# Performance work log

Measured on AMD Instinct MI355X. Metric: run time of the kernel, lower is better.

Reference implementation:

```python
import jax, jax.numpy as jnp
import numpy as np

GROUPS = 32
HEADS = 8
EPS = 1e-5


def setup_inputs() -> dict:
    key = jax.random.key(0)
    ks = jax.random.split(key, 3)
    b, c, h, w = 8, 512, 32, 32
    x = jax.random.normal(ks[0], (b, c, h, w), dtype=jnp.float32)
    gn_w = jnp.ones((c,), jnp.float32)
    gn_b = jnp.zeros((c,), jnp.float32)
    qkv_w = jax.random.normal(ks[1], (3 * c, c), dtype=jnp.float32) * (1.0 / np.sqrt(c))
    qkv_b = jnp.zeros((3 * c,), jnp.float32)
    proj_w = jax.random.normal(ks[2], (c, c), dtype=jnp.float32) * (1.0 / np.sqrt(c))
    proj_b = jnp.zeros((c,), jnp.float32)
    return {"x": x, "gn_w": gn_w, "gn_b": gn_b, "qkv_w": qkv_w,
            "qkv_b": qkv_b, "proj_w": proj_w, "proj_b": proj_b}


def group_norm(x, weight, bias):
    b, c, h, w = x.shape
    xg = x.reshape(b, GROUPS, c // GROUPS, h, w)
    mean = xg.mean(axis=(2, 3, 4), keepdims=True)
    var = xg.var(axis=(2, 3, 4), keepdims=True)
    xn = ((xg - mean) * jax.lax.rsqrt(var + EPS)).reshape(b, c, h, w)
    return xn * weight[None, :, None, None] + bias[None, :, None, None]


def reference(x, gn_w, gn_b, qkv_w, qkv_b, proj_w, proj_b):
    b, c, h, w = x.shape
    dh = c // HEADS
    xn = group_norm(x, gn_w, gn_b)
    # 1x1 conv == per-pixel linear: (b,c,h,w) x (3c,c) -> (b,3c,h,w)
    qkv = jnp.einsum('bchw,oc->bohw', xn, qkv_w) + qkv_b[None, :, None, None]
    qkv = qkv.reshape(b, 3, HEADS, dh, h * w)  # 'three' outermost, then heads, head_dim
    q, k, v = qkv[:, 0], qkv[:, 1], qkv[:, 2]  # (b, heads, dh, hw)
    scale = dh ** (-0.5)
    attn = jax.nn.softmax(jnp.einsum('bhci,bhcj->bhij', q, k) * scale, axis=-1)
    out = jnp.einsum('bhij,bhcj->bhci', attn, v)  # (b, heads, dh, hw)
    out = out.reshape(b, c, h, w)
    out = jnp.einsum('bchw,oc->bohw', out, proj_w) + proj_b[None, :, None, None]
    return x + out
```

## Files before the change

### kernel.cpp

```cpp
#include <hip/hip_runtime.h>
#include <cstdint>
#include <cstddef>

#define BATCH 8
#define CCH   512
#define SSP   1024
#define NH    8
#define DH    64
#define O3    1536

typedef __bf16 bf16x8 __attribute__((ext_vector_type(8)));
typedef float  f32x4  __attribute__((ext_vector_type(4)));

__device__ __forceinline__ unsigned short f2bf(float f) {
    unsigned u = __builtin_bit_cast(unsigned, f);
    unsigned r = u + 0x7fffu + ((u >> 16) & 1u);
    return (unsigned short)(r >> 16);
}

__device__ __forceinline__ unsigned pk2bf(float lo, float hi) {
    unsigned ul = __builtin_bit_cast(unsigned, lo) + 0x8000u;
    unsigned uh = __builtin_bit_cast(unsigned, hi) + 0x8000u;
    return __builtin_amdgcn_perm(uh, ul, 0x07060302u);
}

__device__ __forceinline__ bf16x8 ld8(const unsigned short* p) {
    uint4 u = *(const uint4*)p;
    return __builtin_bit_cast(bf16x8, u);
}

__device__ __forceinline__ void glls16(const void* g, void* l) {
    __builtin_amdgcn_global_load_lds(
        (const __attribute__((address_space(1))) unsigned*)g,
        (__attribute__((address_space(3))) unsigned*)l, 16, 0, 0);
}

__global__ __launch_bounds__(256) void gn_wconv(const float* __restrict__ x,
                                                const float* __restrict__ gw,
                                                const float* __restrict__ gb,
                                                unsigned short* __restrict__ xnt,
                                                const float* __restrict__ s1,
                                                unsigned short* __restrict__ d1, int n1,
                                                const float* __restrict__ s2,
                                                unsigned short* __restrict__ d2) {
    int t = threadIdx.x;
    if (blockIdx.x >= 256) {
        int i = (blockIdx.x - 256) * 256 + t;
        const float4* sp;
        ushort4* dp;
        if (i < n1) { sp = (const float4*)s1 + i; dp = (ushort4*)d1 + i; }
        else        { sp = (const float4*)s2 + (i - n1); dp = (ushort4*)d2 + (i - n1); }
        float4 v = *sp;
        ushort4 o;
        o.x = f2bf(v.x); o.y = f2bf(v.y); o.z = f2bf(v.z); o.w = f2bf(v.w);
        *dp = o;
        return;
    }

    int blk = blockIdx.x;
    int b = blk >> 5, g = blk & 31;
    const float4* xp = (const float4*)(x + (size_t)(b * CCH + g * 16) * SSP);

    float4 vals[16];
    float sum = 0.f, ss = 0.f;
#pragma unroll
    for (int i = 0; i < 16; i++) {
        float4 v = xp[i * 256 + t];
        vals[i] = v;
        sum += (v.x + v.y) + (v.z + v.w);
        ss  += (v.x * v.x + v.y * v.y) + (v.z * v.z + v.w * v.w);
    }
#pragma unroll
    for (int o = 32; o; o >>= 1) {
        sum += __shfl_xor(sum, o, 64);
        ss  += __shfl_xor(ss,  o, 64);
    }
    __shared__ float red[8];
    if ((t & 63) == 0) { red[(t >> 6) * 2] = sum; red[(t >> 6) * 2 + 1] = ss; }
    __syncthreads();
    sum = red[0] + red[2] + red[4] + red[6];
    ss  = red[1] + red[3] + red[5] + red[7];

    float mean = sum * (1.f / 16384.f);
    float var  = ss * (1.f / 16384.f) - mean * mean;
    float rstd = rsqrtf(var + 1e-5f);

    __shared__ unsigned short tile[16][1032];
#pragma unroll
    for (int i = 0; i < 16; i++) {
        int f4 = i * 256 + t;
        int c = f4 >> 8;
        int s = (f4 & 255) * 4;
        float wsc = gw[g * 16 + c] * rstd;
        float bia = gb[g * 16 + c] - mean * wsc;
        float4 v = vals[i];
        tile[c][s + 0] = f2bf(v.x * wsc + bia);
        tile[c][s + 1] = f2bf(v.y * wsc + bia);
        tile[c][s + 2] = f2bf(v.z * wsc + bia);
        tile[c][s + 3] = f2bf(v.w * wsc + bia);
    }
    __syncthreads();

    int c2 = (t & 7) * 2, sr = t >> 3;
    unsigned short* outbase = xnt + (size_t)b * SSP * CCH + g * 16 + c2;
#pragma unroll
    for (int i = 0; i < 32; i++) {
        int s = i * 32 + sr;
        unsigned v = (unsigned)tile[c2][s] | ((unsigned)tile[c2 + 1][s] << 16);
        *(unsigned*)(outbase + (size_t)s * CCH) = v;
    }
}

__global__ __launch_bounds__(256) void gemm_qkv(const unsigned short* __restrict__ Aall,
                                                const unsigned short* __restrict__ Bw,
                                                const float* __restrict__ bias,
                                                unsigned short* __restrict__ Call,
                                                unsigned short* __restrict__ vtout) {
    const int K = 512;
    int bz = blockIdx.z;
    const unsigned short* A = Aall + (size_t)bz * SSP * CCH;
    int m0 = blockIdx.x * 128, n0 = blockIdx.y * 128;

    __shared__ unsigned short As[128 * 64], Bs[128 * 64];
    int t = threadIdx.x, wave = t >> 6, lane = t & 63;
    int quad = lane >> 4, l16 = lane & 15;
    int wm = (wave & 1) * 64, wn = (wave >> 1) * 64;

    int lrow = lane >> 3;
    int lc   = ((lane & 7) - lrow) & 7;
    const unsigned short* Ag = A  + (size_t)(m0 + wave * 32 + lrow) * K + lc * 8;
    const unsigned short* Bg = Bw + (size_t)(n0 + wave * 32 + lrow) * K + lc * 8;
    unsigned short* Asw = As + wave * 2048;
    unsigned short* Bsw = Bs + wave * 2048;

    f32x4 acc[4][4];
#pragma unroll
    for (int i = 0; i < 4; i++)
#pragma unroll
        for (int j = 0; j < 4; j++) acc[i][j] = f32x4{0.f, 0.f, 0.f, 0.f};

    int rowA = (wm + l16) * 64, rowB = (wn + l16) * 64;
    int cph[2];
#pragma unroll
    for (int kc = 0; kc < 2; kc++) cph[kc] = ((quad + 4 * kc + l16) & 7) * 8;

    for (int k0 = 0; k0 < K; k0 += 64) {
        __syncthreads();
#pragma unroll
        for (int i = 0; i < 4; i++) {
            glls16(Ag + (size_t)i * 8 * K + k0, Asw + i * 512);
            glls16(Bg + (size_t)i * 8 * K + k0, Bsw + i * 512);
        }
        __syncthreads();
#pragma unroll
        for (int kc = 0; kc < 2; kc++) {
            bf16x8 af[4], bfr[4];
#pragma unroll
            for (int i = 0; i < 4; i++) {
                af[i]  = ld8(As + rowA + i * 1024 + cph[kc]);
                bfr[i] = ld8(Bs + rowB + i * 1024 + cph[kc]);
            }
#pragma unroll
            for (int i = 0; i < 4; i++)
#pragma unroll
                for (int j = 0; j < 4; j++)
                    acc[i][j] = __builtin_amdgcn_mfma_f32_16x16x32_bf16(af[i], bfr[j], acc[i][j], 0, 0, 0);
        }
    }

    if (n0 < 1024) {
        float scl = (n0 < 512) ? 0.18033688011f : 1.0f;
        unsigned short* Cp = Call + (size_t)bz * SSP * O3;
#pragma unroll
        for (int i = 0; i < 4; i++)
#pragma unroll
            for (int j = 0; j < 4; j++) {
                int col = n0 + wn + j * 16 + l16;
                float bv = bias[col];
#pragma unroll
                for (int r = 0; r < 4; r++) {
                    int row = m0 + wm + i * 16 + quad * 4 + r;
                    Cp[(size_t)row * O3 + col] = f2bf((acc[i][j][r] + bv) * scl);
                }
            }
    } else {
#pragma unroll
        for (int j = 0; j < 4; j++) {
            int col = n0 + wn + j * 16 + l16;
            float bv = bias[col];
            unsigned short* vp = vtout + ((size_t)bz * 512 + (col - 1024)) * SSP;
#pragma unroll
            for (int i = 0; i < 4; i++) {
                int s = m0 + wm + i * 16 + quad * 4;
                uint2 d;
                d.x = pk2bf(acc[i][j][0] + bv, acc[i][j][1] + bv);
                d.y = pk2bf(acc[i][j][2] + bv, acc[i][j][3] + bv);
                *(uint2*)(vp + s) = d;
            }
        }
    }
}

__global__ __launch_bounds__(256) void gemm_proj(const unsigned short* __restrict__ Pw,
                                                 const unsigned short* __restrict__ Oall,
                                                 const float* __restrict__ bias,
                                                 const float* __restrict__ xres,
                                                 float* __restrict__ Out) {
    const int K = 512;
    int bz = blockIdx.z;
    const unsigned short* Bv = Oall + (size_t)bz * SSP * CCH;
    int m0 = blockIdx.x * 64, n0 = blockIdx.y * 128;

    __shared__ unsigned short As[64 * 64], Bs[128 * 64];
    int t = threadIdx.x, wave = t >> 6, lane = t & 63;
    int quad = lane >> 4, l16 = lane & 15;
    int wr = (wave & 1) * 32, wc = (wave >> 1) * 64;

    int lrow = lane >> 3;
    int lc   = ((lane & 7) - lrow) & 7;
    const unsigned short* Ag = Pw + (size_t)(m0 + wave * 16 + lrow) * K + lc * 8;
    const unsigned short* Bg = Bv + (size_t)(n0 + wave * 32 + lrow) * K + lc * 8;
    unsigned short* Asw = As + wave * 1024;
    unsigned short* Bsw = Bs + wave * 2048;

    f32x4 acc[2][4];
#pragma unroll
    for (int i = 0; i < 2; i++)
#pragma unroll
        for (int j = 0; j < 4; j++) acc[i][j] = f32x4{0.f, 0.f, 0.f, 0.f};

    int rowA = (wr + l16) * 64, rowB = (wc + l16) * 64;
    int cph[2];
#pragma unroll
    for (int kc = 0; kc < 2; kc++) cph[kc] = ((quad + 4 * kc + l16) & 7) * 8;

    for (int k0 = 0; k0 < K; k0 += 64) {
        __syncthreads();
#pragma unroll
        for (int i = 0; i < 2; i++)
            glls16(Ag + (size_t)i * 8 * K + k0, Asw + i * 512);
#pragma unroll
        for (int i = 0; i < 4; i++)
            glls16(Bg + (size_t)i * 8 * K + k0, Bsw + i * 512);
        __syncthreads();
#pragma unroll
        for (int kc = 0; kc < 2; kc++) {
            bf16x8 af[2], bfr[4];
#pragma unroll
            for (int i = 0; i < 2; i++) af[i]  = ld8(As + rowA + i * 1024 + cph[kc]);
#pragma unroll
            for (int j = 0; j < 4; j++) bfr[j] = ld8(Bs + rowB + j * 1024 + cph[kc]);
#pragma unroll
            for (int i = 0; i < 2; i++)
#pragma unroll
                for (int j = 0; j < 4; j++)
                    acc[i][j] = __builtin_amdgcn_mfma_f32_16x16x32_bf16(af[i], bfr[j], acc[i][j], 0, 0, 0);
        }
    }
#pragma unroll
    for (int i = 0; i < 2; i++)
#pragma unroll
        for (int j = 0; j < 4; j++) {
            int col = n0 + wc + j * 16 + l16;
#pragma unroll
            for (int r = 0; r < 4; r++) {
                int row = m0 + wr + i * 16 + quad * 4 + r;
                size_t idx = (size_t)bz * CCH * SSP + (size_t)row * SSP + col;
                Out[idx] = xres[idx] + acc[i][j][r] + bias[row];
            }
        }
}

__global__ __launch_bounds__(256, 4) void attn(const unsigned short* __restrict__ qkvt,
                                               const unsigned short* __restrict__ vt,
                                               unsigned short* __restrict__ ot) {
    int blk = blockIdx.x;
    int xcd = blk & 7, jj = blk >> 3;
    int bh = xcd * 8 + (jj >> 4);
    int i0 = (jj & 15) * 64;
    int b = bh >> 3, h = bh & 7;

    __shared__ unsigned short KsD[2][64 * 64];
    __shared__ unsigned short VsD[2][64 * 64];
    __shared__ unsigned short PsD[4][16 * 64];

    int t = threadIdx.x, wave = t >> 6, lane = t & 63;
    int quad = lane >> 4, l16 = lane & 15;

    unsigned short* Ps = PsD[wave];

    bf16x8 qf[2];
    {
        const unsigned short* qp =
            qkvt + ((size_t)b * SSP + i0 + wave * 16 + l16) * O3 + h * DH + quad * 8;
        qf[0] = ld8(qp);
        qf[1] = ld8(qp + 32);
    }

    f32x4 Oa[4];
#pragma unroll
    for (int i = 0; i < 4; i++) Oa[i] = f32x4{0.f, 0.f, 0.f, 0.f};
    float l_acc = 0.f;

    int lrow8 = lane >> 3, lc8 = ((lane & 7) - lrow8) & 7;
    const unsigned short* kga = qkvt + (size_t)b * SSP * O3 + CCH + h * DH;
    const unsigned short* vga = vt + (size_t)bh * DH * SSP;
    size_t koff[2];
    int voff[2], lds_off[2];
#pragma unroll
    for (int p = 0; p < 2; p++) {
        int row = wave * 16 + p * 8 + lrow8;
        koff[p] = (size_t)row * O3 + lc8 * 8;
        voff[p] = row * SSP + lc8 * 8;
        lds_off[p] = (wave * 16 + p * 8) * 64;
    }

#pragma unroll
    for (int p = 0; p < 2; p++) glls16(kga + koff[p], &KsD[0][lds_off[p]]);
#pragma unroll
    for (int p = 0; p < 2; p++) glls16(vga + voff[p], &VsD[0][lds_off[p]]);
    __syncthreads();

    for (int jb = 0; jb < 16; jb++) {
        int cur = jb & 1;
        if (jb < 15) {
            int nxt = cur ^ 1;
            size_t j1k = (size_t)(jb + 1) * 64 * O3;
            int j1v = (jb + 1) * 64;
#pragma unroll
            for (int p = 0; p < 2; p++) glls16(kga + j1k + koff[p], &KsD[nxt][lds_off[p]]);
#pragma unroll
            for (int p = 0; p < 2; p++) glls16(vga + j1v + voff[p], &VsD[nxt][lds_off[p]]);
        }
        const unsigned short* ks = KsD[cur];
        const unsigned short* vs = VsD[cur];

        f32x4 sc[4];
#pragma unroll
        for (int tj = 0; tj < 4; tj++) sc[tj] = f32x4{0.f, 0.f, 0.f, 0.f};
#pragma unroll
        for (int kc = 0; kc < 2; kc++)
#pragma unroll
            for (int tj = 0; tj < 4; tj++) {
                int row = tj * 16 + l16;
                bf16x8 kf = ld8(ks + row * 64 + ((kc * 4 + quad + l16) & 7) * 8);
                sc[tj] = __builtin_amdgcn_mfma_f32_16x16x32_bf16(kf, qf[kc], sc[tj], 0, 0, 0);
            }

#pragma unroll
        for (int tj = 0; tj < 4; tj++)
#pragma unroll
            for (int r = 0; r < 4; r++) {
                float p = __builtin_amdgcn_exp2f(sc[tj][r]);
                sc[tj][r] = p;
                l_acc += p;
            }

#pragma unroll
        for (int tj = 0; tj < 4; tj++) {
            uint2 d;
            d.x = pk2bf(sc[tj][0], sc[tj][1]);
            d.y = pk2bf(sc[tj][2], sc[tj][3]);
            int phys = (tj * 2 + (quad >> 1) + l16) & 7;
            *(uint2*)(Ps + l16 * 64 + phys * 8 + (quad & 1) * 4) = d;
        }

#pragma unroll
        for (int kj = 0; kj < 2; kj++) {
            bf16x8 pf = ld8(Ps + l16 * 64 + ((kj * 4 + quad + l16) & 7) * 8);
#pragma unroll
            for (int tc = 0; tc < 4; tc++) {
                int row = tc * 16 + l16;
                bf16x8 vf = ld8(vs + row * 64 + ((kj * 4 + quad + l16) & 7) * 8);
                Oa[tc] = __builtin_amdgcn_mfma_f32_16x16x32_bf16(vf, pf, Oa[tc], 0, 0, 0);
            }
        }

        __syncthreads();
    }

    l_acc += __shfl_xor(l_acc, 16, 64);
    l_acc += __shfl_xor(l_acc, 32, 64);
    float rl = 1.f / l_acc;

    int i = i0 + wave * 16 + l16;
    unsigned short* ob = ot + ((size_t)b * SSP + i) * CCH + h * DH;
#pragma unroll
    for (int tc = 0; tc < 4; tc++) {
        uint2 d;
        d.x = pk2bf(Oa[tc][0] * rl, Oa[tc][1] * rl);
        d.y = pk2bf(Oa[tc][2] * rl, Oa[tc][3] * rl);
        *(uint2*)(ob + tc * 16 + quad * 4) = d;
    }
}

extern "C" void kernel_launch(void* const* d_in, const int* in_sizes, int n_in,
                              void* d_out, int out_size, void* d_ws, size_t ws_size,
                              hipStream_t stream) {
    const float* x      = (const float*)d_in[0];
    const float* gn_w   = (const float*)d_in[1];
    const float* gn_b   = (const float*)d_in[2];
    const float* qkv_w  = (const float*)d_in[3];
    const float* qkv_b  = (const float*)d_in[4];
    const float* proj_w = (const float*)d_in[5];
    const float* proj_b = (const float*)d_in[6];
    float* out = (float*)d_out;

    char* ws = (char*)d_ws;
    unsigned short* xnt   = (unsigned short*)(ws);
    unsigned short* qw_bf = (unsigned short*)(ws + 8388608);
    unsigned short* pw_bf = (unsigned short*)(ws + 9961472);
    unsigned short* qkvt  = (unsigned short*)(ws + 10485760);
    unsigned short* vt    = (unsigned short*)(ws + 35651584);
    unsigned short* otb   = (unsigned short*)(ws + 44040192);

    gn_wconv<<<dim3(1280), dim3(256), 0, stream>>>(x, gn_w, gn_b, xnt,
                                                   qkv_w, qw_bf, 196608, proj_w, pw_bf);
    gemm_qkv<<<dim3(8, 12, 8), dim3(256), 0, stream>>>(xnt, qw_bf, qkv_b, qkvt, vt);
    attn<<<dim3(1024), dim3(256), 0, stream>>>(qkvt, vt, otb);
    gemm_proj<<<dim3(8, 8, 8), dim3(256), 0, stream>>>(pw_bf, otb, proj_b, x, out);
}
```

Before: 155.0 us.

## Load K/V fragments directly to registers and process two query subtiles per wave

Replaces the LDS double-buffered K/V staging in the attention kernel with direct global-to-register fragment loads. Each wave now handles 32 query rows as two 16-row subtiles that share the loaded K/V fragments, and the grid is halved. This removes the block-wide barriers and the LDS read traffic for K/V. In exchange, each wave fetches the full K/V tiles from global memory, so L2 traffic rises, the async prefetch overlap is lost, and register use grows.

```diff
diff --git a/kernel.cpp b/kernel.cpp
--- a/kernel.cpp
+++ b/kernel.cpp
@@ -271,126 +271,110 @@
         }
 }
 
-__global__ __launch_bounds__(256, 4) void attn(const unsigned short* __restrict__ qkvt,
+__global__ __launch_bounds__(256, 2) void attn(const unsigned short* __restrict__ qkvt,
                                                const unsigned short* __restrict__ vt,
                                                unsigned short* __restrict__ ot) {
     int blk = blockIdx.x;
     int xcd = blk & 7, jj = blk >> 3;
-    int bh = xcd * 8 + (jj >> 4);
-    int i0 = (jj & 15) * 64;
+    int bh = xcd * 8 + (jj >> 3);
+    int i0 = (jj & 7) * 128;
     int b = bh >> 3, h = bh & 7;
 
-    __shared__ unsigned short KsD[2][64 * 64];
-    __shared__ unsigned short VsD[2][64 * 64];
-    __shared__ unsigned short PsD[4][16 * 64];
+    __shared__ unsigned short PsD[4][2][16 * 64];
 
     int t = threadIdx.x, wave = t >> 6, lane = t & 63;
     int quad = lane >> 4, l16 = lane & 15;
 
-    unsigned short* Ps = PsD[wave];
-
-    bf16x8 qf[2];
-    {
+    bf16x8 qf[2][2];
+#pragma unroll
+    for (int is = 0; is < 2; is++) {
         const unsigned short* qp =
-            qkvt + ((size_t)b * SSP + i0 + wave * 16 + l16) * O3 + h * DH + quad * 8;
-        qf[0] = ld8(qp);
-        qf[1] = ld8(qp + 32);
-    }
-
-    f32x4 Oa[4];
-#pragma unroll
-    for (int i = 0; i < 4; i++) Oa[i] = f32x4{0.f, 0.f, 0.f, 0.f};
-    float l_acc = 0.f;
-
-    int lrow8 = lane >> 3, lc8 = ((lane & 7) - lrow8) & 7;
-    const unsigned short* kga = qkvt + (size_t)b * SSP * O3 + CCH + h * DH;
-    const unsigned short* vga = vt + (size_t)bh * DH * SSP;
-    size_t koff[2];
-    int voff[2], lds_off[2];
-#pragma unroll
-    for (int p = 0; p < 2; p++) {
-        int row = wave * 16 + p * 8 + lrow8;
-        koff[p] = (size_t)row * O3 + lc8 * 8;
-        voff[p] = row * SSP + lc8 * 8;
-        lds_off[p] = (wave * 16 + p * 8) * 64;
-    }
-
-#pragma unroll
-    for (int p = 0; p < 2; p++) glls16(kga + koff[p], &KsD[0][lds_off[p]]);
-#pragma unroll
-    for (int p = 0; p < 2; p++) glls16(vga + voff[p], &VsD[0][lds_off[p]]);
-    __syncthreads();
-
-    for (int jb = 0; jb < 16; jb++) {
-        int cur = jb & 1;
-        if (jb < 15) {
-            int nxt = cur ^ 1;
-            size_t j1k = (size_t)(jb + 1) * 64 * O3;
-            int j1v = (jb + 1) * 64;
-#pragma unroll
-            for (int p = 0; p < 2; p++) glls16(kga + j1k + koff[p], &KsD[nxt][lds_off[p]]);
-#pragma unroll
-            for (int p = 0; p < 2; p++) glls16(vga + j1v + voff[p], &VsD[nxt][lds_off[p]]);
-        }
-        const unsigned short* ks = KsD[cur];
-        const unsigned short* vs = VsD[cur];
-
-        f32x4 sc[4];
-#pragma unroll
-        for (int tj = 0; tj < 4; tj++) sc[tj] = f32x4{0.f, 0.f, 0.f, 0.f};
+            qkvt + ((size_t)b * SSP + i0 + wave * 32 + is * 16 + l16) * O3 + h * DH + quad * 8;
+        qf[0][is] = ld8(qp);
+        qf[1][is] = ld8(qp + 32);
+    }
+
+    f32x4 Oa[2][4];
+#pragma unroll
+    for (int is = 0; is < 2; is++)
+#pragma unroll
+        for (int i = 0; i < 4; i++) Oa[is][i] = f32x4{0.f, 0.f, 0.f, 0.f};
+    float l_acc[2] = {0.f, 0.f};
+
+    const unsigned short* kbase = qkvt + (size_t)b * SSP * O3 + CCH + h * DH;
+    const unsigned short* vbase = vt + (size_t)bh * DH * SSP;
+
+    for (int jt = 0; jt < 16; jt++) {
+        int j0 = jt * 64;
+
+        bf16x8 kf[2][4];
 #pragma unroll
         for (int kc = 0; kc < 2; kc++)
 #pragma unroll
+            for (int tj = 0; tj < 4; tj++)
+                kf[kc][tj] = ld8(kbase + (size_t)(j0 + tj * 16 + l16) * O3 + kc * 32 + quad * 8);
+        bf16x8 vfr[2][4];
+#pragma unroll
+        for (int kj = 0; kj < 2; kj++)
+#pragma unroll
+            for (int tc = 0; tc < 4; tc++)
+                vfr[kj][tc] = ld8(vbase + (tc * 16 + l16) * SSP + j0 + kj * 32 + quad * 8);
+
+#pragma unroll
+        for (int is = 0; is < 2; is++) {
+            f32x4 sc[4];
+#pragma unroll
+            for (int tj = 0; tj < 4; tj++) sc[tj] = f32x4{0.f, 0.f, 0.f, 0.f};
+#pragma unroll
+            for (int kc = 0; kc < 2; kc++)
+#pragma unroll
+                for (int tj = 0; tj < 4; tj++)
+                    sc[tj] = __builtin_amdgcn_mfma_f32_16x16x32_bf16(kf[kc][tj], qf[kc][is], sc[tj], 0, 0, 0);
+
+#pragma unroll
+            for (int tj = 0; tj < 4; tj++)
+#pragma unroll
+                for (int r = 0; r < 4; r++) {
+                    float p = __builtin_amdgcn_exp2f(sc[tj][r]);
+                    sc[tj][r] = p;
+                    l_acc[is] += p;
+                }
+
+            unsigned short* Ps = PsD[wave][is];
+#pragma unroll
             for (int tj = 0; tj < 4; tj++) {
-                int row = tj * 16 + l16;
-                bf16x8 kf = ld8(ks + row * 64 + ((kc * 4 + quad + l16) & 7) * 8);
-                sc[tj] = __builtin_amdgcn_mfma_f32_16x16x32_bf16(kf, qf[kc], sc[tj], 0, 0, 0);
-            }
-
-#pragma unroll
-        for (int tj = 0; tj < 4; tj++)
-#pragma unroll
-            for (int r = 0; r < 4; r++) {
-                float p = __builtin_amdgcn_exp2f(sc[tj][r]);
-                sc[tj][r] = p;
-                l_acc += p;
-            }
-
-#pragma unroll
-        for (int tj = 0; tj < 4; tj++) {
+                uint2 d;
+                d.x = pk2bf(sc[tj][0], sc[tj][1]);
+                d.y = pk2bf(sc[tj][2], sc[tj][3]);
+                int phys = (tj * 2 + (quad >> 1) + l16) & 7;
+                *(uint2*)(Ps + l16 * 64 + phys * 8 + (quad & 1) * 4) = d;
+            }
+
+#pragma unroll
+            for (int kj = 0; kj < 2; kj++) {
+                bf16x8 pf = ld8(Ps + l16 * 64 + ((kj * 4 + quad + l16) & 7) * 8);
+#pragma unroll
+                for (int tc = 0; tc < 4; tc++)
+                    Oa[is][tc] = __builtin_amdgcn_mfma_f32_16x16x32_bf16(vfr[kj][tc], pf, Oa[is][tc], 0, 0, 0);
+            }
+        }
+    }
+
+#pragma unroll
+    for (int is = 0; is < 2; is++) {
+        float l = l_acc[is];
+        l += __shfl_xor(l, 16, 64);
+        l += __shfl_xor(l, 32, 64);
+        float rl = 1.f / l;
+        int i = i0 + wave * 32 + is * 16 + l16;
+        unsigned short* ob = ot + ((size_t)b * SSP + i) * CCH + h * DH;
+#pragma unroll
+        for (int tc = 0; tc < 4; tc++) {
             uint2 d;
-            d.x = pk2bf(sc[tj][0], sc[tj][1]);
-            d.y = pk2bf(sc[tj][2], sc[tj][3]);
-            int phys = (tj * 2 + (quad >> 1) + l16) & 7;
-            *(uint2*)(Ps + l16 * 64 + phys * 8 + (quad & 1) * 4) = d;
-        }
-
-#pragma unroll
-        for (int kj = 0; kj < 2; kj++) {
-            bf16x8 pf = ld8(Ps + l16 * 64 + ((kj * 4 + quad + l16) & 7) * 8);
-#pragma unroll
-            for (int tc = 0; tc < 4; tc++) {
-                int row = tc * 16 + l16;
-                bf16x8 vf = ld8(vs + row * 64 + ((kj * 4 + quad + l16) & 7) * 8);
-                Oa[tc] = __builtin_amdgcn_mfma_f32_16x16x32_bf16(vf, pf, Oa[tc], 0, 0, 0);
-            }
-        }
-
-        __syncthreads();
-    }
-
-    l_acc += __shfl_xor(l_acc, 16, 64);
-    l_acc += __shfl_xor(l_acc, 32, 64);
-    float rl = 1.f / l_acc;
-
-    int i = i0 + wave * 16 + l16;
-    unsigned short* ob = ot + ((size_t)b * SSP + i) * CCH + h * DH;
-#pragma unroll
-    for (int tc = 0; tc < 4; tc++) {
-        uint2 d;
-        d.x = pk2bf(Oa[tc][0] * rl, Oa[tc][1] * rl);
-        d.y = pk2bf(Oa[tc][2] * rl, Oa[tc][3] * rl);
-        *(uint2*)(ob + tc * 16 + quad * 4) = d;
+            d.x = pk2bf(Oa[is][tc][0] * rl, Oa[is][tc][1] * rl);
+            d.y = pk2bf(Oa[is][tc][2] * rl, Oa[is][tc][3] * rl);
+            *(uint2*)(ob + tc * 16 + quad * 4) = d;
+        }
     }
 }
 
@@ -417,6 +401,6 @@
     gn_wconv<<<dim3(1280), dim3(256), 0, stream>>>(x, gn_w, gn_b, xnt,
                                                    qkv_w, qw_bf, 196608, proj_w, pw_bf);
     gemm_qkv<<<dim3(8, 12, 8), dim3(256), 0, stream>>>(xnt, qw_bf, qkv_b, qkvt, vt);
-    attn<<<dim3(1024), dim3(256), 0, stream>>>(qkvt, vt, otb);
+    attn<<<dim3(512), dim3(256), 0, stream>>>(qkvt, vt, otb);
     gemm_proj<<<dim3(8, 8, 8), dim3(256), 0, stream>>>(pw_bf, otb, proj_b, x, out);
 }
```

After: 187.3 us. 20.8% more time.
